# Performance work log

Measured on AMD Instinct MI355X. Metric: run time of the kernel, lower is better.

The kernel has to match this reference:

```python
import jax, jax.numpy as jnp
import numpy as np
from jax import lax

STD_H, STD_W = 364, 280
RADIUS, SIGMA = 15, 4.0


def gaussian_kernel():
    r = jnp.arange(-RADIUS, RADIUS + 1, dtype=jnp.float32)
    d2 = r[:, None] ** 2 + r[None, :] ** 2
    k = jnp.exp(-0.5 / (SIGMA ** 2) * d2)
    k = k / k.sum()
    return k[None, None]  # (1,1,31,31) OIHW


def setup_inputs() -> dict:
    key = jax.random.key(0)
    k1, k2 = jax.random.split(key)
    B, H, W = 32, 512, 512
    input_face = jax.random.uniform(k1, (B, 3, H, W), dtype=jnp.float32)
    # landmarks in (x, y) pixel coords within the HxW image
    landmarks = jax.random.uniform(k2, (B, 68, 2), dtype=jnp.float32) * jnp.array([W, H], jnp.float32)
    weight = gaussian_kernel()
    return {"input_face": input_face, "landmarks": landmarks, "weight": weight}


def _blur(x, weight):
    # x: (B,1,h,w), 31x31 'same' conv (kernel symmetric, so corr == conv)
    return lax.conv_general_dilated(x, weight, (1, 1), 'SAME',
                                    dimension_numbers=('NCHW', 'OIHW', 'NCHW'))


def reference(input_face, landmarks, weight):
    B, C, H, W = input_face.shape
    scaling = STD_H / H
    lm = landmarks * scaling                      # (B,68,2) in standard coords
    center = lm[:, 30:31, :]                      # (B,1,2)

    p0 = lm[:, 30:36, :]
    p1 = lm[:, 2:15, :]
    p2 = lm[:, 48:68, :]
    p3 = lm[:, 6:11, :]
    p01 = (p0 - center) * 1.5 + center
    p11 = (p1 - center) * 0.5 + center
    p12 = (p1 - center) * 0.7 + center
    p13 = (p1 - center) * 0.9 + center
    p21 = (p2 - center) * 1.3 + center
    keys = jnp.concatenate([p0, p01, p12, p13, p11, p2, p3, p21], axis=-2)  # (B,96,2)

    iy = jnp.round(jnp.clip(keys[..., 1], 0, STD_H - 1)).astype(jnp.int32)
    ix = jnp.round(jnp.clip(keys[..., 0], 0, STD_W - 1)).astype(jnp.int32)

    # Faithful to torch advanced-indexing semantics: union of ALL batches'
    # points is written into every batch's heatmap.
    hm = jnp.zeros((STD_H, STD_W), jnp.float32).at[iy.ravel(), ix.ravel()].set(1.0)
    hm = jnp.broadcast_to(hm[None, None], (B, 1, STD_H, STD_W))

    w1 = _blur(hm, weight)
    w2 = jnp.where(w1 > 1e-7, 1.0, w1)
    w3 = _blur(w2, weight)

    w_mask = jax.image.resize(w3, (B, 1, H, W), method='bilinear')
    return (1.0 - w_mask) * input_face  # filling='black'
```

## Files before the change

### kernel.cpp

```cpp
#include <hip/hip_runtime.h>

#define BB   32
#define CH   3
#define HH   512
#define WW   512
#define SH   364
#define SW   280
#define RAD  15
#define NK   96
#define HMN  (SH*SW)
#define OMN  (HH*WW)

#define TS   32
#define K1R  (TS + 2*RAD)
#define OH   48
#define OW   64
#define NRMX 36
#define NCMX 37

typedef float f4 __attribute__((ext_vector_type(4)));

__device__ __forceinline__ float gauss_w(int d) {
    return expf(-0.03125f * (float)(d * d));
}

__device__ __forceinline__ void point_ij(const float* __restrict__ lm, int b, int j,
                                         int& ix, int& iy) {
    int idx; float s;
    if      (j <  6) { idx = 30 + j;        s = 1.0f; }
    else if (j < 12) { idx = 30 + (j - 6);  s = 1.5f; }
    else if (j < 25) { idx =  2 + (j - 12); s = 0.7f; }
    else if (j < 38) { idx =  2 + (j - 25); s = 0.9f; }
    else if (j < 51) { idx =  2 + (j - 38); s = 0.5f; }
    else if (j < 71) { idx = 48 + (j - 51); s = 1.0f; }
    else if (j < 76) { idx =  6 + (j - 71); s = 1.0f; }
    else             { idx = 48 + (j - 76); s = 1.3f; }
    const float scal = 364.0f / 512.0f;
    float lx = lm[b * 136 + idx * 2 + 0] * scal;
    float ly = lm[b * 136 + idx * 2 + 1] * scal;
    float kx, ky;
    if (s == 1.0f) { kx = lx; ky = ly; }
    else {
        float cx = lm[b * 136 + 30 * 2 + 0] * scal;
        float cy = lm[b * 136 + 30 * 2 + 1] * scal;
        kx = (lx - cx) * s + cx;
        ky = (ly - cy) * s + cy;
    }
    ix = __float2int_rn(fminf(fmaxf(kx, 0.0f), (float)(SW - 1)));
    iy = __float2int_rn(fminf(fmaxf(ky, 0.0f), (float)(SH - 1)));
}

__global__ __launch_bounds__(256) void k_blur1(const float* __restrict__ lm,
                                               float* __restrict__ w2) {
    __shared__ float hm[K1R][K1R];
    __shared__ float tmp[K1R][TS];
    const int r0 = blockIdx.y * TS, c0 = blockIdx.x * TS;
    const int tid = threadIdx.x;

    for (int i = tid; i < K1R * K1R; i += 256) ((float*)hm)[i] = 0.0f;
    __syncthreads();

    for (int p = tid; p < BB * NK; p += 256) {
        int b = p / NK, j = p - b * NK;
        int ix, iy;
        point_ij(lm, b, j, ix, iy);
        int ly = iy - (r0 - RAD), lx = ix - (c0 - RAD);
        if (ly >= 0 && ly < K1R && lx >= 0 && lx < K1R) hm[ly][lx] = 1.0f;
    }
    __syncthreads();

    for (int i = tid; i < K1R * TS; i += 256) {
        int yy = i / TS, x = i - yy * TS;
        float acc = 0.0f, s1 = 0.0f;
        #pragma unroll
        for (int d = -RAD; d <= RAD; ++d) {
            float g = gauss_w(d);
            s1 += g;
            acc += g * hm[yy][x + RAD + d];
        }
        tmp[yy][x] = acc / s1;
    }
    __syncthreads();

    for (int i = tid; i < TS * TS; i += 256) {
        int y = i / TS, x = i - y * TS;
        int gy = r0 + y, gx = c0 + x;
        if (gy >= SH || gx >= SW) continue;
        float acc = 0.0f, s1 = 0.0f;
        #pragma unroll
        for (int d = -RAD; d <= RAD; ++d) {
            float g = gauss_w(d);
            s1 += g;
            acc += g * tmp[y + RAD + d][x];
        }
        float v = acc / s1;
        w2[gy * SW + gx] = (v > 1e-7f) ? 1.0f : v;
    }
}

__global__ __launch_bounds__(256) void k_blur2_mask(const float* __restrict__ w2,
                                                    float* __restrict__ om) {
    __shared__ float w2r[NRMX + 2*RAD][NCMX + 2*RAD];
    __shared__ float tmp[NRMX + 2*RAD][NCMX];
    __shared__ float w3r[NRMX][NCMX];
    const int h0 = blockIdx.y * OH, w0 = blockIdx.x * OW;
    const int hl = min(h0 + OH - 1, HH - 1), wl = min(w0 + OW - 1, WW - 1);
    const int tid = threadIdx.x;
    const float sy = (float)SH / (float)HH;
    const float sx = (float)SW / (float)WW;

    float fy0 = fmaxf(((float)h0 + 0.5f) * sy - 0.5f, 0.0f);
    float fyl = fminf(((float)hl + 0.5f) * sy - 0.5f, (float)(SH - 1));
    int rbase = (int)fy0;
    int rend  = min(SH - 1, (int)fyl + 1);
    int NR = rend - rbase + 1;
    float fx0 = fmaxf(((float)w0 + 0.5f) * sx - 0.5f, 0.0f);
    float fxl = fminf(((float)wl + 0.5f) * sx - 0.5f, (float)(SW - 1));
    int cbase = (int)fx0;
    int cend  = min(SW - 1, (int)fxl + 1);
    int NC = cend - cbase + 1;
    int SR = NR + 2 * RAD, SC = NC + 2 * RAD;

    for (int i = tid; i < SR * SC; i += 256) {
        int y = i / SC, x = i - y * SC;
        int gy = rbase - RAD + y, gx = cbase - RAD + x;
        float v = 0.0f;
        if (gy >= 0 && gy < SH && gx >= 0 && gx < SW) v = w2[gy * SW + gx];
        w2r[y][x] = v;
    }
    __syncthreads();

    for (int i = tid; i < SR * NC; i += 256) {
        int yy = i / NC, x = i - yy * NC;
        float acc = 0.0f, s1 = 0.0f;
        #pragma unroll
        for (int d = -RAD; d <= RAD; ++d) {
            float g = gauss_w(d);
            s1 += g;
            acc += g * w2r[yy][x + RAD + d];
        }
        tmp[yy][x] = acc / s1;
    }
    __syncthreads();

    for (int i = tid; i < NR * NC; i += 256) {
        int y = i / NC, x = i - y * NC;
        float acc = 0.0f, s1 = 0.0f;
        #pragma unroll
        for (int d = -RAD; d <= RAD; ++d) {
            float g = gauss_w(d);
            s1 += g;
            acc += g * tmp[y + RAD + d][x];
        }
        w3r[y][x] = acc / s1;
    }
    __syncthreads();

    for (int i = tid; i < OH * OW; i += 256) {
        int dh = i / OW, dw = i - dh * OW;
        int h = h0 + dh, w = w0 + dw;
        if (h >= HH || w >= WW) continue;
        float fy = fminf(fmaxf(((float)h + 0.5f) * sy - 0.5f, 0.0f), (float)(SH - 1));
        float fx = fminf(fmaxf(((float)w + 0.5f) * sx - 0.5f, 0.0f), (float)(SW - 1));
        int y0 = (int)fy, x0 = (int)fx;
        int y1 = min(y0 + 1, SH - 1), x1 = min(x0 + 1, SW - 1);
        float ty = fy - (float)y0, tx = fx - (float)x0;
        int ly0 = y0 - rbase, ly1 = y1 - rbase;
        int lx0 = x0 - cbase, lx1 = x1 - cbase;
        float v00 = w3r[ly0][lx0], v01 = w3r[ly0][lx1];
        float v10 = w3r[ly1][lx0], v11 = w3r[ly1][lx1];
        float v = (1.0f - ty) * ((1.0f - tx) * v00 + tx * v01)
                +         ty  * ((1.0f - tx) * v10 + tx * v11);
        om[h * WW + w] = 1.0f - v;
    }
}

__global__ __launch_bounds__(256) void k_final(const f4* __restrict__ in,
                                               const f4* __restrict__ om,
                                               f4* __restrict__ out, int n4) {
    int i = blockIdx.x * blockDim.x + threadIdx.x;
    if (i >= n4) return;
    f4 a = __builtin_nontemporal_load(&in[i]);
    f4 m = om[i & (OMN / 4 - 1)];
    f4 r = a * m;
    __builtin_nontemporal_store(r, &out[i]);
}

extern "C" void kernel_launch(void* const* d_in, const int* in_sizes, int n_in,
                              void* d_out, int out_size, void* d_ws, size_t ws_size,
                              hipStream_t stream) {
    const float* face = (const float*)d_in[0];
    const float* lm   = (const float*)d_in[1];

    float* ws = (float*)d_ws;
    float* w2 = ws;
    float* om = ws + HMN;

    k_blur1<<<dim3((SW + TS - 1) / TS, (SH + TS - 1) / TS), 256, 0, stream>>>(lm, w2);
    k_blur2_mask<<<dim3(WW / OW, (HH + OH - 1) / OH), 256, 0, stream>>>(w2, om);
    int n4 = out_size / 4;
    k_final<<<(n4 + 255) / 256, 256, 0, stream>>>(
        (const f4*)face, (const f4*)om, (f4*)d_out, n4);
}
```

Before: 61.33 us.

## Fuse both blur passes and resize into one tiled mask kernel

Merges the two blur kernels into a single kernel. Each small output tile recomputes the heatmap scatter, the first blur with threshold over a doubled halo, and the second blur in shared memory, which removes the intermediate global buffer and one launch. The separable Gaussian taps now come from the supplied weight tensor and are cached in registers instead of calling expf per tap. The final multiply kernel becomes grid-stride so each thread loads its mask vector once and reuses it across batch and channel. The trade-off is redundant halo computation across the many small tiles.

```diff
diff --git a/kernel.cpp b/kernel.cpp
--- a/kernel.cpp
+++ b/kernel.cpp
@@ -1,28 +1,24 @@
 #include <hip/hip_runtime.h>
 
 #define BB   32
-#define CH   3
 #define HH   512
 #define WW   512
 #define SH   364
 #define SW   280
 #define RAD  15
 #define NK   96
-#define HMN  (SH*SW)
 #define OMN  (HH*WW)
 
-#define TS   32
-#define K1R  (TS + 2*RAD)
-#define OH   48
-#define OW   64
-#define NRMX 36
-#define NCMX 37
+#define OH   16
+#define OW   32
+#define NRM  13
+#define NCM  19
+#define WRM  (NRM + 2*RAD)
+#define WCM  (NCM + 2*RAD)
+#define HRM  (NRM + 4*RAD)
+#define HCM  (NCM + 4*RAD)
 
 typedef float f4 __attribute__((ext_vector_type(4)));
-
-__device__ __forceinline__ float gauss_w(int d) {
-    return expf(-0.03125f * (float)(d * d));
-}
 
 __device__ __forceinline__ void point_ij(const float* __restrict__ lm, int b, int j,
                                          int& ix, int& iy) {
@@ -50,116 +46,93 @@
     iy = __float2int_rn(fminf(fmaxf(ky, 0.0f), (float)(SH - 1)));
 }
 
-__global__ __launch_bounds__(256) void k_blur1(const float* __restrict__ lm,
-                                               float* __restrict__ w2) {
-    __shared__ float hm[K1R][K1R];
-    __shared__ float tmp[K1R][TS];
-    const int r0 = blockIdx.y * TS, c0 = blockIdx.x * TS;
+__global__ __launch_bounds__(256) void k_mask(const float* __restrict__ lm,
+                                              const float* __restrict__ wt,
+                                              float* __restrict__ om) {
+    __shared__ float gwl[31];
+    __shared__ float hmS[HRM][HCM];
+    __shared__ float t1 [HRM][WCM];
+    __shared__ float w2S[WRM][WCM];
+    __shared__ float t2 [WRM][NCM];
+    __shared__ float w3S[NRM][NCM];
+
     const int tid = threadIdx.x;
+    const int h0 = blockIdx.y * OH, w0 = blockIdx.x * OW;
+    const float sy = (float)SH / (float)HH;
+    const float sx = (float)SW / (float)WW;
 
-    for (int i = tid; i < K1R * K1R; i += 256) ((float*)hm)[i] = 0.0f;
+    if (tid < 31) gwl[tid] = wt[15 * 31 + tid] / sqrtf(wt[15 * 31 + 15]);
+
+    const int hl = h0 + OH - 1, wl = w0 + OW - 1;
+    float fy0 = fmaxf(((float)h0 + 0.5f) * sy - 0.5f, 0.0f);
+    float fyl = fminf(((float)hl + 0.5f) * sy - 0.5f, (float)(SH - 1));
+    int rbase = (int)fy0;
+    int rend  = min(SH - 1, (int)fyl + 1);
+    float fx0 = fmaxf(((float)w0 + 0.5f) * sx - 0.5f, 0.0f);
+    float fxl = fminf(((float)wl + 0.5f) * sx - 0.5f, (float)(SW - 1));
+    int cbase = (int)fx0;
+    int cend  = min(SW - 1, (int)fxl + 1);
+    int NR = rend - rbase + 1;
+    int NC = cend - cbase + 1;
+    int HR = NR + 4 * RAD, HC = NC + 4 * RAD;
+
+    for (int i = tid; i < HRM * HCM; i += 256) ((float*)hmS)[i] = 0.0f;
     __syncthreads();
+
+    float g[31];
+    #pragma unroll
+    for (int k = 0; k < 31; ++k) g[k] = gwl[k];
 
     for (int p = tid; p < BB * NK; p += 256) {
         int b = p / NK, j = p - b * NK;
         int ix, iy;
         point_ij(lm, b, j, ix, iy);
-        int ly = iy - (r0 - RAD), lx = ix - (c0 - RAD);
-        if (ly >= 0 && ly < K1R && lx >= 0 && lx < K1R) hm[ly][lx] = 1.0f;
+        int ly = iy - (rbase - 2 * RAD), lx = ix - (cbase - 2 * RAD);
+        if (ly >= 0 && ly < HR && lx >= 0 && lx < HC) hmS[ly][lx] = 1.0f;
     }
     __syncthreads();
 
-    for (int i = tid; i < K1R * TS; i += 256) {
-        int yy = i / TS, x = i - yy * TS;
-        float acc = 0.0f, s1 = 0.0f;
+    for (int i = tid; i < HRM * WCM; i += 256) {
+        int y = i / WCM, x = i - y * WCM;
+        float acc = 0.0f;
         #pragma unroll
-        for (int d = -RAD; d <= RAD; ++d) {
-            float g = gauss_w(d);
-            s1 += g;
-            acc += g * hm[yy][x + RAD + d];
-        }
-        tmp[yy][x] = acc / s1;
+        for (int d = 0; d < 31; ++d) acc += g[d] * hmS[y][x + d];
+        t1[y][x] = acc;
     }
     __syncthreads();
 
-    for (int i = tid; i < TS * TS; i += 256) {
-        int y = i / TS, x = i - y * TS;
-        int gy = r0 + y, gx = c0 + x;
-        if (gy >= SH || gx >= SW) continue;
-        float acc = 0.0f, s1 = 0.0f;
+    for (int i = tid; i < WRM * WCM; i += 256) {
+        int y = i / WCM, x = i - y * WCM;
+        float acc = 0.0f;
         #pragma unroll
-        for (int d = -RAD; d <= RAD; ++d) {
-            float g = gauss_w(d);
-            s1 += g;
-            acc += g * tmp[y + RAD + d][x];
-        }
-        float v = acc / s1;
-        w2[gy * SW + gx] = (v > 1e-7f) ? 1.0f : v;
-    }
-}
-
-__global__ __launch_bounds__(256) void k_blur2_mask(const float* __restrict__ w2,
-                                                    float* __restrict__ om) {
-    __shared__ float w2r[NRMX + 2*RAD][NCMX + 2*RAD];
-    __shared__ float tmp[NRMX + 2*RAD][NCMX];
-    __shared__ float w3r[NRMX][NCMX];
-    const int h0 = blockIdx.y * OH, w0 = blockIdx.x * OW;
-    const int hl = min(h0 + OH - 1, HH - 1), wl = min(w0 + OW - 1, WW - 1);
-    const int tid = threadIdx.x;
-    const float sy = (float)SH / (float)HH;
-    const float sx = (float)SW / (float)WW;
-
-    float fy0 = fmaxf(((float)h0 + 0.5f) * sy - 0.5f, 0.0f);
-    float fyl = fminf(((float)hl + 0.5f) * sy - 0.5f, (float)(SH - 1));
-    int rbase = (int)fy0;
-    int rend  = min(SH - 1, (int)fyl + 1);
-    int NR = rend - rbase + 1;
-    float fx0 = fmaxf(((float)w0 + 0.5f) * sx - 0.5f, 0.0f);
-    float fxl = fminf(((float)wl + 0.5f) * sx - 0.5f, (float)(SW - 1));
-    int cbase = (int)fx0;
-    int cend  = min(SW - 1, (int)fxl + 1);
-    int NC = cend - cbase + 1;
-    int SR = NR + 2 * RAD, SC = NC + 2 * RAD;
-
-    for (int i = tid; i < SR * SC; i += 256) {
-        int y = i / SC, x = i - y * SC;
+        for (int d = 0; d < 31; ++d) acc += g[d] * t1[y + d][x];
+        float v = (acc > 1e-7f) ? 1.0f : acc;
         int gy = rbase - RAD + y, gx = cbase - RAD + x;
-        float v = 0.0f;
-        if (gy >= 0 && gy < SH && gx >= 0 && gx < SW) v = w2[gy * SW + gx];
-        w2r[y][x] = v;
+        w2S[y][x] = (gy >= 0 && gy < SH && gx >= 0 && gx < SW) ? v : 0.0f;
     }
     __syncthreads();
 
-    for (int i = tid; i < SR * NC; i += 256) {
-        int yy = i / NC, x = i - yy * NC;
-        float acc = 0.0f, s1 = 0.0f;
+    for (int i = tid; i < WRM * NCM; i += 256) {
+        int y = i / NCM, x = i - y * NCM;
+        float acc = 0.0f;
         #pragma unroll
-        for (int d = -RAD; d <= RAD; ++d) {
-            float g = gauss_w(d);
-            s1 += g;
-            acc += g * w2r[yy][x + RAD + d];
-        }
-        tmp[yy][x] = acc / s1;
+        for (int d = 0; d < 31; ++d) acc += g[d] * w2S[y][x + d];
+        t2[y][x] = acc;
     }
     __syncthreads();
 
-    for (int i = tid; i < NR * NC; i += 256) {
-        int y = i / NC, x = i - y * NC;
-        float acc = 0.0f, s1 = 0.0f;
+    for (int i = tid; i < NRM * NCM; i += 256) {
+        int y = i / NCM, x = i - y * NCM;
+        float acc = 0.0f;
         #pragma unroll
-        for (int d = -RAD; d <= RAD; ++d) {
-            float g = gauss_w(d);
-            s1 += g;
-            acc += g * tmp[y + RAD + d][x];
-        }
-        w3r[y][x] = acc / s1;
+        for (int d = 0; d < 31; ++d) acc += g[d] * t2[y + d][x];
+        w3S[y][x] = acc;
     }
     __syncthreads();
 
     for (int i = tid; i < OH * OW; i += 256) {
         int dh = i / OW, dw = i - dh * OW;
         int h = h0 + dh, w = w0 + dw;
-        if (h >= HH || w >= WW) continue;
         float fy = fminf(fmaxf(((float)h + 0.5f) * sy - 0.5f, 0.0f), (float)(SH - 1));
         float fx = fminf(fmaxf(((float)w + 0.5f) * sx - 0.5f, 0.0f), (float)(SW - 1));
         int y0 = (int)fy, x0 = (int)fx;
@@ -167,8 +140,8 @@
         float ty = fy - (float)y0, tx = fx - (float)x0;
         int ly0 = y0 - rbase, ly1 = y1 - rbase;
         int lx0 = x0 - cbase, lx1 = x1 - cbase;
-        float v00 = w3r[ly0][lx0], v01 = w3r[ly0][lx1];
-        float v10 = w3r[ly1][lx0], v11 = w3r[ly1][lx1];
+        float v00 = w3S[ly0][lx0], v01 = w3S[ly0][lx1];
+        float v10 = w3S[ly1][lx0], v11 = w3S[ly1][lx1];
         float v = (1.0f - ty) * ((1.0f - tx) * v00 + tx * v01)
                 +         ty  * ((1.0f - tx) * v10 + tx * v11);
         om[h * WW + w] = 1.0f - v;
@@ -178,12 +151,13 @@
 __global__ __launch_bounds__(256) void k_final(const f4* __restrict__ in,
                                                const f4* __restrict__ om,
                                                f4* __restrict__ out, int n4) {
-    int i = blockIdx.x * blockDim.x + threadIdx.x;
-    if (i >= n4) return;
-    f4 a = __builtin_nontemporal_load(&in[i]);
-    f4 m = om[i & (OMN / 4 - 1)];
-    f4 r = a * m;
-    __builtin_nontemporal_store(r, &out[i]);
+    const int i0 = blockIdx.x * 256 + threadIdx.x;
+    f4 m = om[i0 & (OMN / 4 - 1)];
+    const int stride = gridDim.x * 256;
+    for (int i = i0; i < n4; i += stride) {
+        f4 a = __builtin_nontemporal_load(&in[i]);
+        __builtin_nontemporal_store(a * m, &out[i]);
+    }
 }
 
 extern "C" void kernel_launch(void* const* d_in, const int* in_sizes, int n_in,
@@ -191,14 +165,12 @@
                               hipStream_t stream) {
     const float* face = (const float*)d_in[0];
     const float* lm   = (const float*)d_in[1];
+    const float* wt   = (const float*)d_in[2];
 
-    float* ws = (float*)d_ws;
-    float* w2 = ws;
-    float* om = ws + HMN;
+    float* om = (float*)d_ws;
 
-    k_blur1<<<dim3((SW + TS - 1) / TS, (SH + TS - 1) / TS), 256, 0, stream>>>(lm, w2);
-    k_blur2_mask<<<dim3(WW / OW, (HH + OH - 1) / OH), 256, 0, stream>>>(w2, om);
+    k_mask<<<dim3(WW / OW, HH / OH), 256, 0, stream>>>(lm, wt, om);
     int n4 = out_size / 4;
-    k_final<<<(n4 + 255) / 256, 256, 0, stream>>>(
+    k_final<<<2048, 256, 0, stream>>>(
         (const f4*)face, (const f4*)om, (f4*)d_out, n4);
 }
```

Result: faster. 58.16 us, median of 2 (-5.2%).
